# Kernel tuning notes

Measured on AMD Instinct MI355X. Metric: run time of the kernel, lower is better.

Reference implementation:

```python
import jax, jax.numpy as jnp
import numpy as np

B, S, H = 2, 1024, 2048
E, I, K = 32, 768, 4


def setup_inputs() -> dict:
    key = jax.random.key(0)
    k1, k2, k3, k4, k5 = jax.random.split(key, 5)
    sH = 1.0 / np.sqrt(H)
    sI = 1.0 / np.sqrt(I)
    return {
        "hidden_states": jax.random.normal(k1, (B, S, H), dtype=jnp.float32),
        "gate_w": jax.random.normal(k2, (E, H), dtype=jnp.float32) * sH,
        "w_gate": jax.random.normal(k3, (E, H, I), dtype=jnp.float32) * sH,
        "w_up": jax.random.normal(k4, (E, H, I), dtype=jnp.float32) * sH,
        "w_down": jax.random.normal(k5, (E, I, H), dtype=jnp.float32) * sI,
        "top_k": K,
    }


def reference(hidden_states, gate_w, w_gate, w_up, w_down, top_k):
    b, s, h = hidden_states.shape
    x = hidden_states.reshape(-1, h)                      # [T, H]
    T = x.shape[0]

    # Router: logits -> softmax over experts -> top-k -> renormalize
    logits = x @ gate_w.T                                 # [T, E]
    probs = jax.nn.softmax(logits, axis=-1)
    topv, topi = jax.lax.top_k(probs, top_k)              # [T, K]
    topv = topv / jnp.sum(topv, axis=-1, keepdims=True)   # norm_topk_prob

    # Dense routing-weight matrix (zero except selected experts) [T, E]
    rw = jnp.zeros((T, probs.shape[-1]), dtype=x.dtype)
    rw = rw.at[jnp.arange(T)[:, None], topi].set(topv)

    # Expert SwiGLU MLPs, computed for all experts then masked-combined
    g = jnp.einsum('th,ehi->eti', x, w_gate)              # [E, T, I]
    u = jnp.einsum('th,ehi->eti', x, w_up)                # [E, T, I]
    act = jax.nn.silu(g) * u                              # [E, T, I]
    expert_out = jnp.einsum('eti,eih->eth', act, w_down)  # [E, T, H]

    out = jnp.einsum('te,eth->th', rw, expert_out)        # combine [T, H]
    return out.reshape(b, s, h).astype(hidden_states.dtype)
```

## Files before the change

kernel.cpp:

```cpp
#include <hip/hip_runtime.h>
#include <hip/hip_bf16.h>
#include <math.h>

typedef unsigned short u16;
typedef unsigned int u32;
typedef unsigned long long u64;
typedef short s16x8 __attribute__((ext_vector_type(8)));
typedef u16 u16x8 __attribute__((ext_vector_type(8)));
typedef u32 u32x2 __attribute__((ext_vector_type(2)));
typedef u32 u32x4 __attribute__((ext_vector_type(4)));
typedef float f32x4 __attribute__((ext_vector_type(4)));

#define TTOK 2048
#define HDIM 2048
#define ENUM 32
#define IDIM 768
#define KTOP 4

#define WS_XB   0L
#define WS_ACT  8388608L
#define WS_TIDX 20971520L
#define WS_TW   (WS_TIDX + 32768L)
#define WS_CNT  (WS_TW + 32768L)
#define WS_OFFS (WS_CNT + 128L)
#define WS_CUR  (WS_OFFS + 256L)
#define WS_RTOK (WS_CUR + 128L)
#define WS_RW   (WS_RTOK + 32768L)
#define WS_RMAP (WS_RW + 32768L)
#define WS_EO   25165824L
#define WS_NEED (WS_EO + 33554432L)

#define LDBW 20

__device__ __forceinline__ u16 f2bf(float f) {
  unsigned u = __builtin_bit_cast(unsigned, f);
  unsigned r = (u + 0x7fffu + ((u >> 16) & 1u)) >> 16;
  return (u16)r;
}

__device__ __forceinline__ u32 cvtpk(float lo, float hi) {
  u32 r;
  asm("v_cvt_pk_bf16_f32 %0, %1, %2" : "=v"(r) : "v"(lo), "v"(hi));
  return r;
}

__device__ __forceinline__ void gll16(const void* g, void* l) {
  u32 loff = __builtin_amdgcn_readfirstlane((u32)(u64)l);
  __builtin_amdgcn_global_load_lds(
      (const __attribute__((address_space(1))) u32*)(u64)g,
      (__attribute__((address_space(3))) u32*)loff, 16, 0, 0);
}

__device__ __forceinline__ s16x8 bfrag(const u32* B, int d0, int d1) {
  u32x2 lo = *(const u32x2*)(B + d0);
  u32x2 hi = *(const u32x2*)(B + d1);
  u32x4 v = {lo.x, lo.y, hi.x, hi.y};
  return __builtin_bit_cast(s16x8, v);
}

#define WAIT_VM(N)                                            \
  do {                                                        \
    asm volatile("s_waitcnt vmcnt(" #N ")");                  \
    __builtin_amdgcn_sched_barrier(0);                        \
  } while (0)
#define BARRIER()                                             \
  do {                                                        \
    asm volatile("s_waitcnt lgkmcnt(0)");                     \
    __builtin_amdgcn_sched_barrier(0);                        \
    __builtin_amdgcn_s_barrier();                             \
    __builtin_amdgcn_sched_barrier(0);                        \
  } while (0)

__global__ __launch_bounds__(256) void router_kernel(const float* __restrict__ x,
                                                     const float* __restrict__ gw,
                                                     u16* __restrict__ xb,
                                                     int* __restrict__ tidx,
                                                     float* __restrict__ tw,
                                                     int* __restrict__ counts) {
  __shared__ float xs[HDIM];
  __shared__ float part[256];
  __shared__ float lg[ENUM];
  int t = blockIdx.x;
  const float4* xr = (const float4*)(x + (long)t * HDIM);
  float4* xs4 = (float4*)xs;
  for (int i = threadIdx.x; i < HDIM / 4; i += 256) xs4[i] = xr[i];
  __syncthreads();
  {
    int i0 = threadIdx.x * 8;
    uint4 o;
    o.x = cvtpk(xs[i0], xs[i0 + 1]);
    o.y = cvtpk(xs[i0 + 2], xs[i0 + 3]);
    o.z = cvtpk(xs[i0 + 4], xs[i0 + 5]);
    o.w = cvtpk(xs[i0 + 6], xs[i0 + 7]);
    *(uint4*)(xb + (long)t * HDIM + i0) = o;
  }
  int e = threadIdx.x >> 3, ch = threadIdx.x & 7;
  const float4* gp = (const float4*)(gw + (long)e * HDIM + ch * 256);
  const float4* xp = (const float4*)(xs + ch * 256);
  float s = 0.f;
#pragma unroll 8
  for (int c = 0; c < 64; c++) {
    float4 gv = gp[c], xv = xp[c];
    s += gv.x * xv.x + gv.y * xv.y + gv.z * xv.z + gv.w * xv.w;
  }
  part[threadIdx.x] = s;
  __syncthreads();
  if (threadIdx.x < 32) {
    float v = 0.f;
#pragma unroll
    for (int j = 0; j < 8; j++) v += part[threadIdx.x * 8 + j];
    lg[threadIdx.x] = v;
  }
  __syncthreads();
  if (threadIdx.x == 0) {
    int sel[KTOP]; float sv[KTOP];
    unsigned mask = 0;
    for (int k = 0; k < KTOP; k++) {
      float best = -INFINITY; int bi = 0;
      for (int j = 0; j < ENUM; j++)
        if (!((mask >> j) & 1u) && lg[j] > best) { best = lg[j]; bi = j; }
      mask |= 1u << bi; sel[k] = bi; sv[k] = best;
    }
    float m = sv[0], den = 0.f, ex[KTOP];
    for (int k = 0; k < KTOP; k++) { ex[k] = expf(sv[k] - m); den += ex[k]; }
    for (int k = 0; k < KTOP; k++) {
      tidx[t * KTOP + k] = sel[k];
      tw[t * KTOP + k] = ex[k] / den;
      atomicAdd(&counts[sel[k]], 1);
    }
  }
}

__global__ void scan_kernel(const int* __restrict__ counts, int* __restrict__ offs,
                            int* __restrict__ cur) {
  if (threadIdx.x == 0) {
    int a = 0;
    for (int e = 0; e < ENUM; e++) { offs[e] = a; a += counts[e]; }
    offs[ENUM] = a;
  }
  if (threadIdx.x < ENUM) cur[threadIdx.x] = 0;
}

__global__ __launch_bounds__(256) void scatter_kernel(const int* __restrict__ tidx,
                                                      const float* __restrict__ tw,
                                                      const int* __restrict__ offs,
                                                      int* __restrict__ cur,
                                                      int* __restrict__ rtok,
                                                      float* __restrict__ rw,
                                                      int* __restrict__ rowmap) {
  int i = blockIdx.x * 256 + threadIdx.x;
  int e = tidx[i];
  int pos = atomicAdd(&cur[e], 1);
  int row = offs[e] + pos;
  rtok[row] = i >> 2;
  rw[row] = tw[i];
  rowmap[i] = row;
}

__global__ __launch_bounds__(512) void gemm1_kernel(const u16* __restrict__ xb,
                                                    const float* __restrict__ wgp,
                                                    const float* __restrict__ wup,
                                                    const int* __restrict__ offs,
                                                    const int* __restrict__ rtok,
                                                    u16* __restrict__ act) {
  int d = blockIdx.x;
  int e = d & 31;
  int nt = (d >> 5) % 12;
  int mt = d / 384;
  int off = offs[e], cnt = offs[e + 1] - off;
  int m0 = mt << 8;
  if (m0 >= cnt) return;
  int rows = cnt - m0; if (rows > 256) rows = 256;
  int baser = off + m0;
  int n0 = nt << 6;

  __shared__ __align__(16) u16 As[3][256 * 32];
  __shared__ __align__(16) u32 Bs[2][2][64 * LDBW];

  int tid = threadIdx.x;
  int ln = tid & 63, w = tid >> 6;
  int wm = w >> 1, wn = w & 1;
  int lhi = ln >> 4, llo = ln & 15;

  const u16* gA[2];
  int ldsA[2];
#pragma unroll
  for (int j = 0; j < 2; j++) {
    int idx = w * 2 + j;
    int r = idx * 16 + (ln >> 2);
    int c = ln & 3;
    int csrc = c ^ ((r >> 1) & 3);
    int rr = r < rows ? r : rows - 1;
    gA[j] = xb + (long)rtok[baser + rr] * HDIM + csrc * 8;
    ldsA[j] = idx * 1024;
  }

  int mat = tid >> 8;
  int t2 = tid & 255;
  int a = t2 & 15;
  int kk = t2 >> 4;
  const float* gB = (mat ? wup : wgp) + (long)e * ((long)HDIM * IDIM) +
                    (long)(2 * kk) * IDIM + n0 + 4 * a;
  int fB = 2 * (a & 7);
  int wOff[4];
#pragma unroll
  for (int j = 0; j < 4; j++) wOff[j] = (4 * a + j) * LDBW + (kk ^ fB);

  int offA[4];
#pragma unroll
  for (int mf = 0; mf < 4; mf++) {
    int r = wm * 64 + mf * 16 + llo;
    offA[mf] = r * 64 + ((lhi ^ ((r >> 1) & 3)) * 16);
  }
  int dB0[2], dB1[2];
#pragma unroll
  for (int nf = 0; nf < 2; nf++) {
    int n = wn * 32 + nf * 16 + llo;
    int f = 2 * ((n >> 2) & 7);
    dB0[nf] = n * LDBW + ((4 * lhi) ^ f);
    dB1[nf] = n * LDBW + (((4 * lhi) | 2) ^ f);
  }

  f32x4 accg[4][2], accu[4][2];
  f32x4 zz = {0.f, 0.f, 0.f, 0.f};
#pragma unroll
  for (int i = 0; i < 4; i++)
#pragma unroll
    for (int j = 0; j < 2; j++) { accg[i][j] = zz; accu[i][j] = zz; }

  float4 rbA0, rbA1, rbB0, rbB1;

#define GLLA(pDst, tt)                                                \
  { gll16(gA[0] + (tt) * 32, (char*)(pDst) + ldsA[0]);                \
    gll16(gA[1] + (tt) * 32, (char*)(pDst) + ldsA[1]); }
#define LDB1(r0, r1, tt)                                              \
  { const float* p = gB + (long)(tt) * 32 * IDIM;                     \
    r0 = *(const float4*)p; r1 = *(const float4*)(p + IDIM); }
#define STB1(dstBs, r0, r1)                                           \
  { u32* bb = &(dstBs)[mat][0];                                       \
    bb[wOff[0]] = cvtpk(r0.x, r1.x);                                  \
    bb[wOff[1]] = cvtpk(r0.y, r1.y);                                  \
    bb[wOff[2]] = cvtpk(r0.z, r1.z);                                  \
    bb[wOff[3]] = cvtpk(r0.w, r1.w); }
#define COMP1(pA, bsel)                                               \
  {                                                                   \
    const char* Ab = (const char*)(pA);                               \
    const u32* Bg = &Bs[bsel][0][0];                                  \
    const u32* Bu = &Bs[bsel][1][0];                                  \
    s16x8 av[4];                                                      \
    _Pragma("unroll")                                                 \
    for (int mf = 0; mf < 4; mf++) av[mf] = *(const s16x8*)(Ab + offA[mf]); \
    _Pragma("unroll")                                                 \
    for (int nf = 0; nf < 2; nf++) {                                  \
      s16x8 bg = bfrag(Bg, dB0[nf], dB1[nf]);                         \
      s16x8 bu = bfrag(Bu, dB0[nf], dB1[nf]);                         \
      _Pragma("unroll")                                               \
      for (int mf = 0; mf < 4; mf++) {                                \
        accg[mf][nf] = __builtin_amdgcn_mfma_f32_16x16x32_bf16(av[mf], bg, accg[mf][nf], 0, 0, 0); \
        accu[mf][nf] = __builtin_amdgcn_mfma_f32_16x16x32_bf16(av[mf], bu, accu[mf][nf], 0, 0, 0); \
      }                                                               \
    }                                                                 \
  }

  const int NS = HDIM / 32;
  u16 *pC = As[0], *pN = As[1], *pD = As[2];

  GLLA(pC, 0); LDB1(rbA0, rbA1, 0);
  GLLA(pN, 1); LDB1(rbB0, rbB1, 1);
  __builtin_amdgcn_sched_barrier(0);
  STB1(Bs[0], rbA0, rbA1);
  WAIT_VM(4);
  BARRIER();

  for (int t = 0; t < NS; t += 2) {
    if (t + 2 < NS) { GLLA(pD, t + 2); LDB1(rbA0, rbA1, t + 2); }
    __builtin_amdgcn_sched_barrier(0);
    COMP1(pC, 0);
    __builtin_amdgcn_sched_barrier(0);
    STB1(Bs[1], rbB0, rbB1);
    if (t + 2 < NS) WAIT_VM(4); else WAIT_VM(0);
    BARRIER();
    { u16* tmp = pC; pC = pN; pN = pD; pD = tmp; }
    if (t + 3 < NS) { GLLA(pD, t + 3); LDB1(rbB0, rbB1, t + 3); }
    __builtin_amdgcn_sched_barrier(0);
    COMP1(pC, 1);
    __builtin_amdgcn_sched_barrier(0);
    if (t + 2 < NS) STB1(Bs[0], rbA0, rbA1);
    if (t + 3 < NS) WAIT_VM(4); else WAIT_VM(0);
    if (t + 2 < NS) BARRIER();
    { u16* tmp = pC; pC = pN; pN = pD; pD = tmp; }
  }

  int rb = wm * 64 + lhi * 4;
  int cb = n0 + wn * 32 + llo;
#pragma unroll
  for (int mf = 0; mf < 4; mf++) {
#pragma unroll
    for (int r4 = 0; r4 < 4; r4++) {
      int rl = rb + mf * 16 + r4;
      if (rl < rows) {
        long rowb = (long)(baser + rl) * IDIM;
#pragma unroll
        for (int nf = 0; nf < 2; nf++) {
          float g = accg[mf][nf][r4], u = accu[mf][nf][r4];
          float av = g / (1.f + __expf(-g)) * u;
          act[rowb + cb + nf * 16] = f2bf(av);
        }
      }
    }
  }
#undef GLLA
#undef LDB1
#undef STB1
#undef COMP1
}

template <int STORE>
__global__ __launch_bounds__(512) void gemm2_kernel(const u16* __restrict__ act,
                                                    const float* __restrict__ wdp,
                                                    const int* __restrict__ offs,
                                                    const int* __restrict__ rtok,
                                                    const float* __restrict__ rw,
                                                    u16* __restrict__ eo,
                                                    float* __restrict__ out) {
  int d = blockIdx.x;
  int e = d & 31;
  int nt = (d >> 5) & 31;
  int mt = d >> 10;
  int off = offs[e], cnt = offs[e + 1] - off;
  int m0 = mt << 8;
  if (m0 >= cnt) return;
  int rows = cnt - m0; if (rows > 256) rows = 256;
  int baser = off + m0;
  int n0 = nt << 6;

  __shared__ __align__(16) u16 As[3][256 * 32];
  __shared__ __align__(16) u32 Bs[2][64 * LDBW];

  int tid = threadIdx.x;
  int ln = tid & 63, w = tid >> 6;
  int wm = w >> 1, wn = w & 1;
  int lhi = ln >> 4, llo = ln & 15;

  const u16* gA[2];
  int ldsA[2];
#pragma unroll
  for (int j = 0; j < 2; j++) {
    int idx = w * 2 + j;
    int r = idx * 16 + (ln >> 2);
    int c = ln & 3;
    int csrc = c ^ ((r >> 1) & 3);
    int rr = r < rows ? r : rows - 1;
    gA[j] = act + (long)(baser + rr) * IDIM + csrc * 8;
    ldsA[j] = idx * 1024;
  }

  int isB = (tid < 256);
  int a = tid & 15;
  int kk = (tid >> 4) & 15;
  const float* gB = wdp + (long)e * ((long)IDIM * HDIM) +
                    (long)(2 * kk) * HDIM + n0 + 4 * a;
  int fB = 2 * (a & 7);
  int wOff[4];
#pragma unroll
  for (int j = 0; j < 4; j++) wOff[j] = (4 * a + j) * LDBW + (kk ^ fB);

  int offA[4];
#pragma unroll
  for (int mf = 0; mf < 4; mf++) {
    int r = wm * 64 + mf * 16 + llo;
    offA[mf] = r * 64 + ((lhi ^ ((r >> 1) & 3)) * 16);
  }
  int dB0[2], dB1[2];
#pragma unroll
  for (int nf = 0; nf < 2; nf++) {
    int n = wn * 32 + nf * 16 + llo;
    int f = 2 * ((n >> 2) & 7);
    dB0[nf] = n * LDBW + ((4 * lhi) ^ f);
    dB1[nf] = n * LDBW + (((4 * lhi) | 2) ^ f);
  }

  f32x4 acc[4][2];
  f32x4 zz = {0.f, 0.f, 0.f, 0.f};
#pragma unroll
  for (int i = 0; i < 4; i++)
#pragma unroll
    for (int j = 0; j < 2; j++) acc[i][j] = zz;

  float4 rbA0, rbA1, rbB0, rbB1;

#define GLLA(pDst, tt)                                                \
  { gll16(gA[0] + (tt) * 32, (char*)(pDst) + ldsA[0]);                \
    gll16(gA[1] + (tt) * 32, (char*)(pDst) + ldsA[1]); }
#define LDB2(r0, r1, tt)                                              \
  { if (isB) {                                                        \
      const float* p = gB + (long)(tt) * 32 * HDIM;                   \
      r0 = *(const float4*)p; r1 = *(const float4*)(p + HDIM); } }
#define STB2(dstBs, r0, r1)                                           \
  { if (isB) {                                                        \
      u32* bb = &(dstBs)[0];                                          \
      bb[wOff[0]] = cvtpk(r0.x, r1.x);                                \
      bb[wOff[1]] = cvtpk(r0.y, r1.y);                                \
      bb[wOff[2]] = cvtpk(r0.z, r1.z);                                \
      bb[wOff[3]] = cvtpk(r0.w, r1.w); } }
#define WAITG2(nB, nNB)                                               \
  { if (isB) WAIT_VM(nB); else WAIT_VM(nNB); }
#define COMP2(pA, bsel)                                               \
  {                                                                   \
    const char* Ab = (const char*)(pA);                               \
    const u32* Bb = &Bs[bsel][0];                                     \
    s16x8 av[4];                                                      \
    _Pragma("unroll")                                                 \
    for (int mf = 0; mf < 4; mf++) av[mf] = *(const s16x8*)(Ab + offA[mf]); \
    _Pragma("unroll")                                                 \
    for (int nf = 0; nf < 2; nf++) {                                  \
      s16x8 bv = bfrag(Bb, dB0[nf], dB1[nf]);                         \
      _Pragma("unroll")                                               \
      for (int mf = 0; mf < 4; mf++)                                  \
        acc[mf][nf] = __builtin_amdgcn_mfma_f32_16x16x32_bf16(av[mf], bv, acc[mf][nf], 0, 0, 0); \
    }                                                                 \
  }

  const int NS = IDIM / 32;
  u16 *pC = As[0], *pN = As[1], *pD = As[2];

  GLLA(pC, 0); LDB2(rbA0, rbA1, 0);
  GLLA(pN, 1); LDB2(rbB0, rbB1, 1);
  __builtin_amdgcn_sched_barrier(0);
  STB2(Bs[0], rbA0, rbA1);
  WAITG2(4, 2);
  BARRIER();

  for (int t = 0; t < NS; t += 2) {
    if (t + 2 < NS) { GLLA(pD, t + 2); LDB2(rbA0, rbA1, t + 2); }
    __builtin_amdgcn_sched_barrier(0);
    COMP2(pC, 0);
    __builtin_amdgcn_sched_barrier(0);
    STB2(Bs[1], rbB0, rbB1);
    if (t + 2 < NS) { WAITG2(4, 2); } else { WAIT_VM(0); }
    BARRIER();
    { u16* tmp = pC; pC = pN; pN = pD; pD = tmp; }
    if (t + 3 < NS) { GLLA(pD, t + 3); LDB2(rbB0, rbB1, t + 3); }
    __builtin_amdgcn_sched_barrier(0);
    COMP2(pC, 1);
    __builtin_amdgcn_sched_barrier(0);
    if (t + 2 < NS) STB2(Bs[0], rbA0, rbA1);
    if (t + 3 < NS) { WAITG2(4, 2); } else { WAIT_VM(0); }
    if (t + 2 < NS) BARRIER();
    { u16* tmp = pC; pC = pN; pN = pD; pD = tmp; }
  }

  int rb = wm * 64 + lhi * 4;
  int cb = n0 + wn * 32 + llo;
#pragma unroll
  for (int mf = 0; mf < 4; mf++) {
#pragma unroll
    for (int r4 = 0; r4 < 4; r4++) {
      int rl = rb + mf * 16 + r4;
      if (rl < rows) {
        int rr = baser + rl;
        if (STORE) {
          long ob = (long)rr * HDIM + cb;
          eo[ob] = f2bf(acc[mf][0][r4]);
          eo[ob + 16] = f2bf(acc[mf][1][r4]);
        } else {
          float wt = rw[rr];
          long ob = (long)rtok[rr] * HDIM + cb;
          atomicAdd(&out[ob], acc[mf][0][r4] * wt);
          atomicAdd(&out[ob + 16], acc[mf][1][r4] * wt);
        }
      }
    }
  }
#undef GLLA
#undef LDB2
#undef STB2
#undef WAITG2
#undef COMP2
}

__global__ __launch_bounds__(256) void combine_kernel(const u16* __restrict__ eo,
                                                      const int* __restrict__ rowmap,
                                                      const float* __restrict__ tw,
                                                      float* __restrict__ out) {
  int t = blockIdx.x;
  int h0 = threadIdx.x * 8;
  float acc[8] = {0.f, 0.f, 0.f, 0.f, 0.f, 0.f, 0.f, 0.f};
#pragma unroll
  for (int k = 0; k < KTOP; k++) {
    int r = rowmap[t * KTOP + k];
    float wt = tw[t * KTOP + k];
    u16x8 v = *(const u16x8*)(eo + (long)r * HDIM + h0);
#pragma unroll
    for (int j = 0; j < 8; j++)
      acc[j] += wt * __builtin_bit_cast(float, ((u32)v[j]) << 16);
  }
  float4 o0 = {acc[0], acc[1], acc[2], acc[3]};
  float4 o1 = {acc[4], acc[5], acc[6], acc[7]};
  *(float4*)(out + (long)t * HDIM + h0) = o0;
  *(float4*)(out + (long)t * HDIM + h0 + 4) = o1;
}

extern "C" void kernel_launch(void* const* d_in, const int* in_sizes, int n_in,
                              void* d_out, int out_size, void* d_ws, size_t ws_size,
                              hipStream_t stream) {
  const float* x = (const float*)d_in[0];
  const float* gw = (const float*)d_in[1];
  const float* wgate = (const float*)d_in[2];
  const float* wup = (const float*)d_in[3];
  const float* wdown = (const float*)d_in[4];
  float* out = (float*)d_out;

  char* ws = (char*)d_ws;
  u16* xb = (u16*)(ws + WS_XB);
  u16* act = (u16*)(ws + WS_ACT);
  int* tidx = (int*)(ws + WS_TIDX);
  float* tw = (float*)(ws + WS_TW);
  int* cnt = (int*)(ws + WS_CNT);
  int* offs = (int*)(ws + WS_OFFS);
  int* cur = (int*)(ws + WS_CUR);
  int* rtok = (int*)(ws + WS_RTOK);
  float* rw = (float*)(ws + WS_RW);
  int* rowmap = (int*)(ws + WS_RMAP);
  u16* eo = (u16*)(ws + WS_EO);
  bool storeMode = (ws_size >= (size_t)WS_NEED);

  hipMemsetAsync(cnt, 0, 128, stream);
  if (!storeMode)
    hipMemsetAsync(d_out, 0, (size_t)out_size * sizeof(float), stream);

  hipLaunchKernelGGL(router_kernel, dim3(TTOK), dim3(256), 0, stream, x, gw, xb, tidx, tw, cnt);
  hipLaunchKernelGGL(scan_kernel, dim3(1), dim3(64), 0, stream, cnt, offs, cur);
  hipLaunchKernelGGL(scatter_kernel, dim3(TTOK * KTOP / 256), dim3(256), 0, stream, tidx, tw, offs, cur, rtok, rw, rowmap);
  hipLaunchKernelGGL(gemm1_kernel, dim3(32 * 12 * 8), dim3(512), 0, stream, xb, wgate, wup, offs, rtok, act);
  if (storeMode) {
    hipLaunchKernelGGL(gemm2_kernel<1>, dim3(32 * 32 * 8), dim3(512), 0, stream, act, wdown, offs, rtok, rw, eo, out);
    hipLaunchKernelGGL(combine_kernel, dim3(TTOK), dim3(256), 0, stream, eo, rowmap, tw, out);
  } else {
    hipLaunchKernelGGL(gemm2_kernel<0>, dim3(32 * 32 * 8), dim3(512), 0, stream, act, wdown, offs, rtok, rw, eo, out);
  }
}
```

Baseline: 444.2 us.

## Switch GEMMs to double-buffered A pipeline and widen gemm2 N-tile to 128

Both expert GEMMs move from a triple-buffered A ring with rotating pointers to a two-buffer ping-pong scheme. A-tile loads are issued one step ahead and B loads two steps ahead, with tighter vmcnt waits. gemm2 now uses a 128-column N tile with all 512 threads loading B, which halves its grid and doubles A reuse per block. The cost is less prefetch depth for A and more accumulator registers in gemm2, which can reduce latency hiding and occupancy.

```diff
diff --git a/kernel.cpp b/kernel.cpp
--- a/kernel.cpp
+++ b/kernel.cpp
@@ -58,18 +58,15 @@
   return __builtin_bit_cast(s16x8, v);
 }
 
-#define WAIT_VM(N)                                            \
-  do {                                                        \
-    asm volatile("s_waitcnt vmcnt(" #N ")");                  \
-    __builtin_amdgcn_sched_barrier(0);                        \
-  } while (0)
-#define BARRIER()                                             \
-  do {                                                        \
-    asm volatile("s_waitcnt lgkmcnt(0)");                     \
-    __builtin_amdgcn_sched_barrier(0);                        \
-    __builtin_amdgcn_s_barrier();                             \
-    __builtin_amdgcn_sched_barrier(0);                        \
-  } while (0)
+#define WTV2 do { asm volatile("s_waitcnt vmcnt(2)" ::: "memory"); \
+                  __builtin_amdgcn_sched_barrier(0); } while (0)
+#define WTV0 do { asm volatile("s_waitcnt vmcnt(0)" ::: "memory"); \
+                  __builtin_amdgcn_sched_barrier(0); } while (0)
+#define BARR do { asm volatile("s_waitcnt lgkmcnt(0)" ::: "memory"); \
+                  __builtin_amdgcn_sched_barrier(0); \
+                  __builtin_amdgcn_s_barrier(); \
+                  __builtin_amdgcn_sched_barrier(0); } while (0)
+#define SBAR __builtin_amdgcn_sched_barrier(0)
 
 __global__ __launch_bounds__(256) void router_kernel(const float* __restrict__ x,
                                                      const float* __restrict__ gw,
@@ -174,7 +171,7 @@
   int baser = off + m0;
   int n0 = nt << 6;
 
-  __shared__ __align__(16) u16 As[3][256 * 32];
+  __shared__ __align__(16) u16 As[2][256 * 32];
   __shared__ __align__(16) u32 Bs[2][2][64 * LDBW];
 
   int tid = threadIdx.x;
@@ -228,23 +225,23 @@
 #pragma unroll
     for (int j = 0; j < 2; j++) { accg[i][j] = zz; accu[i][j] = zz; }
 
-  float4 rbA0, rbA1, rbB0, rbB1;
-
-#define GLLA(pDst, tt)                                                \
-  { gll16(gA[0] + (tt) * 32, (char*)(pDst) + ldsA[0]);                \
-    gll16(gA[1] + (tt) * 32, (char*)(pDst) + ldsA[1]); }
+  float4 pa0, pa1, pb0, pb1;
+
+#define GLL1(buf, tt)                                                 \
+  { gll16(gA[0] + (tt) * 32, (char*)As[buf] + ldsA[0]);               \
+    gll16(gA[1] + (tt) * 32, (char*)As[buf] + ldsA[1]); }
 #define LDB1(r0, r1, tt)                                              \
   { const float* p = gB + (long)(tt) * 32 * IDIM;                     \
     r0 = *(const float4*)p; r1 = *(const float4*)(p + IDIM); }
-#define STB1(dstBs, r0, r1)                                           \
-  { u32* bb = &(dstBs)[mat][0];                                       \
+#define STB1(bsel, r0, r1)                                            \
+  { u32* bb = &Bs[bsel][mat][0];                                      \
     bb[wOff[0]] = cvtpk(r0.x, r1.x);                                  \
     bb[wOff[1]] = cvtpk(r0.y, r1.y);                                  \
     bb[wOff[2]] = cvtpk(r0.z, r1.z);                                  \
     bb[wOff[3]] = cvtpk(r0.w, r1.w); }
-#define COMP1(pA, bsel)                                               \
+#define COMP1(bsel)                                                   \
   {                                                                   \
-    const char* Ab = (const char*)(pA);                               \
+    const char* Ab = (const char*)As[bsel];                           \
     const u32* Bg = &Bs[bsel][0][0];                                  \
     const u32* Bu = &Bs[bsel][1][0];                                  \
     s16x8 av[4];                                                      \
@@ -263,32 +260,35 @@
   }
 
   const int NS = HDIM / 32;
-  u16 *pC = As[0], *pN = As[1], *pD = As[2];
-
-  GLLA(pC, 0); LDB1(rbA0, rbA1, 0);
-  GLLA(pN, 1); LDB1(rbB0, rbB1, 1);
-  __builtin_amdgcn_sched_barrier(0);
-  STB1(Bs[0], rbA0, rbA1);
-  WAIT_VM(4);
-  BARRIER();
+  LDB1(pa0, pa1, 0);
+  GLL1(0, 0);
+  LDB1(pb0, pb1, 1);
+  SBAR;
+  STB1(0, pa0, pa1);
+  WTV2;
+  BARR;
 
   for (int t = 0; t < NS; t += 2) {
-    if (t + 2 < NS) { GLLA(pD, t + 2); LDB1(rbA0, rbA1, t + 2); }
-    __builtin_amdgcn_sched_barrier(0);
-    COMP1(pC, 0);
-    __builtin_amdgcn_sched_barrier(0);
-    STB1(Bs[1], rbB0, rbB1);
-    if (t + 2 < NS) WAIT_VM(4); else WAIT_VM(0);
-    BARRIER();
-    { u16* tmp = pC; pC = pN; pN = pD; pD = tmp; }
-    if (t + 3 < NS) { GLLA(pD, t + 3); LDB1(rbB0, rbB1, t + 3); }
-    __builtin_amdgcn_sched_barrier(0);
-    COMP1(pC, 1);
-    __builtin_amdgcn_sched_barrier(0);
-    if (t + 2 < NS) STB1(Bs[0], rbA0, rbA1);
-    if (t + 3 < NS) WAIT_VM(4); else WAIT_VM(0);
-    if (t + 2 < NS) BARRIER();
-    { u16* tmp = pC; pC = pN; pN = pD; pD = tmp; }
+    if (t + 1 < NS) GLL1(1, t + 1);
+    SBAR;
+    if (t + 2 < NS) LDB1(pa0, pa1, t + 2);
+    SBAR;
+    COMP1(0);
+    if (t + 1 < NS) STB1(1, pb0, pb1);
+    if (t + 2 < NS) { WTV2; } else { WTV0; }
+    BARR;
+    if (t + 2 < NS) {
+      GLL1(0, t + 2);
+      SBAR;
+      if (t + 3 < NS) LDB1(pb0, pb1, t + 3);
+      SBAR;
+      COMP1(1);
+      STB1(0, pa0, pa1);
+      if (t + 3 < NS) { WTV2; } else { WTV0; }
+      BARR;
+    } else {
+      COMP1(1);
+    }
   }
 
   int rb = wm * 64 + lhi * 4;
@@ -309,7 +309,7 @@
       }
     }
   }
-#undef GLLA
+#undef GLL1
 #undef LDB1
 #undef STB1
 #undef COMP1
@@ -325,17 +325,17 @@
                                                     float* __restrict__ out) {
   int d = blockIdx.x;
   int e = d & 31;
-  int nt = (d >> 5) & 31;
-  int mt = d >> 10;
+  int nt = (d >> 5) & 15;
+  int mt = d >> 9;
   int off = offs[e], cnt = offs[e + 1] - off;
   int m0 = mt << 8;
   if (m0 >= cnt) return;
   int rows = cnt - m0; if (rows > 256) rows = 256;
   int baser = off + m0;
-  int n0 = nt << 6;
-
-  __shared__ __align__(16) u16 As[3][256 * 32];
-  __shared__ __align__(16) u32 Bs[2][64 * LDBW];
+  int n0 = nt << 7;
+
+  __shared__ __align__(16) u16 As[2][256 * 32];
+  __shared__ __align__(16) u32 Bs[2][128 * LDBW];
 
   int tid = threadIdx.x;
   int ln = tid & 63, w = tid >> 6;
@@ -355,9 +355,8 @@
     ldsA[j] = idx * 1024;
   }
 
-  int isB = (tid < 256);
-  int a = tid & 15;
-  int kk = (tid >> 4) & 15;
+  int a = tid & 31;
+  int kk = (tid >> 5) & 15;
   const float* gB = wdp + (long)e * ((long)IDIM * HDIM) +
                     (long)(2 * kk) * HDIM + n0 + 4 * a;
   int fB = 2 * (a & 7);
@@ -371,49 +370,45 @@
     int r = wm * 64 + mf * 16 + llo;
     offA[mf] = r * 64 + ((lhi ^ ((r >> 1) & 3)) * 16);
   }
-  int dB0[2], dB1[2];
-#pragma unroll
-  for (int nf = 0; nf < 2; nf++) {
-    int n = wn * 32 + nf * 16 + llo;
+  int dB0[4], dB1[4];
+#pragma unroll
+  for (int nf = 0; nf < 4; nf++) {
+    int n = wn * 64 + nf * 16 + llo;
     int f = 2 * ((n >> 2) & 7);
     dB0[nf] = n * LDBW + ((4 * lhi) ^ f);
     dB1[nf] = n * LDBW + (((4 * lhi) | 2) ^ f);
   }
 
-  f32x4 acc[4][2];
+  f32x4 acc[4][4];
   f32x4 zz = {0.f, 0.f, 0.f, 0.f};
 #pragma unroll
   for (int i = 0; i < 4; i++)
 #pragma unroll
-    for (int j = 0; j < 2; j++) acc[i][j] = zz;
-
-  float4 rbA0, rbA1, rbB0, rbB1;
-
-#define GLLA(pDst, tt)                                                \
-  { gll16(gA[0] + (tt) * 32, (char*)(pDst) + ldsA[0]);                \
-    gll16(gA[1] + (tt) * 32, (char*)(pDst) + ldsA[1]); }
+    for (int j = 0; j < 4; j++) acc[i][j] = zz;
+
+  float4 pa0, pa1, pb0, pb1;
+
+#define GLL2(buf, tt)                                                 \
+  { gll16(gA[0] + (tt) * 32, (char*)As[buf] + ldsA[0]);               \
+    gll16(gA[1] + (tt) * 32, (char*)As[buf] + ldsA[1]); }
 #define LDB2(r0, r1, tt)                                              \
-  { if (isB) {                                                        \
-      const float* p = gB + (long)(tt) * 32 * HDIM;                   \
-      r0 = *(const float4*)p; r1 = *(const float4*)(p + HDIM); } }
-#define STB2(dstBs, r0, r1)                                           \
-  { if (isB) {                                                        \
-      u32* bb = &(dstBs)[0];                                          \
-      bb[wOff[0]] = cvtpk(r0.x, r1.x);                                \
-      bb[wOff[1]] = cvtpk(r0.y, r1.y);                                \
-      bb[wOff[2]] = cvtpk(r0.z, r1.z);                                \
-      bb[wOff[3]] = cvtpk(r0.w, r1.w); } }
-#define WAITG2(nB, nNB)                                               \
-  { if (isB) WAIT_VM(nB); else WAIT_VM(nNB); }
-#define COMP2(pA, bsel)                                               \
+  { const float* p = gB + (long)(tt) * 32 * HDIM;                     \
+    r0 = *(const float4*)p; r1 = *(const float4*)(p + HDIM); }
+#define STB2(bsel, r0, r1)                                            \
+  { u32* bb = &Bs[bsel][0];                                           \
+    bb[wOff[0]] = cvtpk(r0.x, r1.x);                                  \
+    bb[wOff[1]] = cvtpk(r0.y, r1.y);                                  \
+    bb[wOff[2]] = cvtpk(r0.z, r1.z);                                  \
+    bb[wOff[3]] = cvtpk(r0.w, r1.w); }
+#define COMP2(bsel)                                                   \
   {                                                                   \
-    const char* Ab = (const char*)(pA);                               \
+    const char* Ab = (const char*)As[bsel];                           \
     const u32* Bb = &Bs[bsel][0];                                     \
     s16x8 av[4];                                                      \
     _Pragma("unroll")                                                 \
     for (int mf = 0; mf < 4; mf++) av[mf] = *(const s16x8*)(Ab + offA[mf]); \
     _Pragma("unroll")                                                 \
-    for (int nf = 0; nf < 2; nf++) {                                  \
+    for (int nf = 0; nf < 4; nf++) {                                  \
       s16x8 bv = bfrag(Bb, dB0[nf], dB1[nf]);                         \
       _Pragma("unroll")                                               \
       for (int mf = 0; mf < 4; mf++)                                  \
@@ -422,36 +417,39 @@
   }
 
   const int NS = IDIM / 32;
-  u16 *pC = As[0], *pN = As[1], *pD = As[2];
-
-  GLLA(pC, 0); LDB2(rbA0, rbA1, 0);
-  GLLA(pN, 1); LDB2(rbB0, rbB1, 1);
-  __builtin_amdgcn_sched_barrier(0);
-  STB2(Bs[0], rbA0, rbA1);
-  WAITG2(4, 2);
-  BARRIER();
+  LDB2(pa0, pa1, 0);
+  GLL2(0, 0);
+  LDB2(pb0, pb1, 1);
+  SBAR;
+  STB2(0, pa0, pa1);
+  WTV2;
+  BARR;
 
   for (int t = 0; t < NS; t += 2) {
-    if (t + 2 < NS) { GLLA(pD, t + 2); LDB2(rbA0, rbA1, t + 2); }
-    __builtin_amdgcn_sched_barrier(0);
-    COMP2(pC, 0);
-    __builtin_amdgcn_sched_barrier(0);
-    STB2(Bs[1], rbB0, rbB1);
-    if (t + 2 < NS) { WAITG2(4, 2); } else { WAIT_VM(0); }
-    BARRIER();
-    { u16* tmp = pC; pC = pN; pN = pD; pD = tmp; }
-    if (t + 3 < NS) { GLLA(pD, t + 3); LDB2(rbB0, rbB1, t + 3); }
-    __builtin_amdgcn_sched_barrier(0);
-    COMP2(pC, 1);
-    __builtin_amdgcn_sched_barrier(0);
-    if (t + 2 < NS) STB2(Bs[0], rbA0, rbA1);
-    if (t + 3 < NS) { WAITG2(4, 2); } else { WAIT_VM(0); }
-    if (t + 2 < NS) BARRIER();
-    { u16* tmp = pC; pC = pN; pN = pD; pD = tmp; }
+    if (t + 1 < NS) GLL2(1, t + 1);
+    SBAR;
+    if (t + 2 < NS) LDB2(pa0, pa1, t + 2);
+    SBAR;
+    COMP2(0);
+    if (t + 1 < NS) STB2(1, pb0, pb1);
+    if (t + 2 < NS) { WTV2; } else { WTV0; }
+    BARR;
+    if (t + 2 < NS) {
+      GLL2(0, t + 2);
+      SBAR;
+      if (t + 3 < NS) LDB2(pb0, pb1, t + 3);
+      SBAR;
+      COMP2(1);
+      STB2(0, pa0, pa1);
+      if (t + 3 < NS) { WTV2; } else { WTV0; }
+      BARR;
+    } else {
+      COMP2(1);
+    }
   }
 
   int rb = wm * 64 + lhi * 4;
-  int cb = n0 + wn * 32 + llo;
+  int cb = n0 + wn * 64 + llo;
 #pragma unroll
   for (int mf = 0; mf < 4; mf++) {
 #pragma unroll
@@ -461,21 +459,22 @@
         int rr = baser + rl;
         if (STORE) {
           long ob = (long)rr * HDIM + cb;
-          eo[ob] = f2bf(acc[mf][0][r4]);
-          eo[ob + 16] = f2bf(acc[mf][1][r4]);
+#pragma unroll
+          for (int nf = 0; nf < 4; nf++)
+            eo[ob + nf * 16] = f2bf(acc[mf][nf][r4]);
         } else {
           float wt = rw[rr];
           long ob = (long)rtok[rr] * HDIM + cb;
-          atomicAdd(&out[ob], acc[mf][0][r4] * wt);
-          atomicAdd(&out[ob + 16], acc[mf][1][r4] * wt);
+#pragma unroll
+          for (int nf = 0; nf < 4; nf++)
+            atomicAdd(&out[ob + nf * 16], acc[mf][nf][r4] * wt);
         }
       }
     }
   }
-#undef GLLA
+#undef GLL2
 #undef LDB2
 #undef STB2
-#undef WAITG2
 #undef COMP2
 }
 
@@ -534,9 +533,9 @@
   hipLaunchKernelGGL(scatter_kernel, dim3(TTOK * KTOP / 256), dim3(256), 0, stream, tidx, tw, offs, cur, rtok, rw, rowmap);
   hipLaunchKernelGGL(gemm1_kernel, dim3(32 * 12 * 8), dim3(512), 0, stream, xb, wgate, wup, offs, rtok, act);
   if (storeMode) {
-    hipLaunchKernelGGL(gemm2_kernel<1>, dim3(32 * 32 * 8), dim3(512), 0, stream, act, wdown, offs, rtok, rw, eo, out);
+    hipLaunchKernelGGL(gemm2_kernel<1>, dim3(32 * 16 * 8), dim3(512), 0, stream, act, wdown, offs, rtok, rw, eo, out);
     hipLaunchKernelGGL(combine_kernel, dim3(TTOK), dim3(256), 0, stream, eo, rowmap, tw, out);
   } else {
-    hipLaunchKernelGGL(gemm2_kernel<0>, dim3(32 * 32 * 8), dim3(512), 0, stream, act, wdown, offs, rtok, rw, eo, out);
-  }
-}
+    hipLaunchKernelGGL(gemm2_kernel<0>, dim3(32 * 16 * 8), dim3(512), 0, stream, act, wdown, offs, rtok, rw, eo, out);
+  }
+}
```

After: 396.8 us. -10.7%, faster.
